# Kernel optimization log

Hardware: AMD Instinct MI355X
Metric: run time of the kernel (lower is better)

Reference implementation:

```python
import jax, jax.numpy as jnp
import numpy as np

# Fixed molemap hierarchy: leaf groups under level-2 nodes 65..72
GROUPS = [(0, 7), (7, 30), (30, 48), (48, 53), (53, 58), (58, 59), (59, 62), (62, 65)]
GROUP_SIZES = [b - a for a, b in GROUPS]
# group index of each leaf (which of nodes 65..72 is its parent)
GIDX = np.repeat(np.arange(8), GROUP_SIZES)
# top branch of each leaf: 0 -> node 73 (leaves 0..52), 1 -> node 74 (leaves 53..64)
TIDX = (np.arange(65) >= 53).astype(np.int32)


def _forward(x):
    # x: [N, 65] leaf logits
    N = x.shape[0]
    # leaf-level probs: softmax of leaf logits within each sibling group (children of 65..72)
    leaf_probs = jnp.concatenate(
        [jax.nn.softmax(x[:, a:b], axis=-1) for a, b in GROUPS], axis=-1
    )  # [N, 65]
    # level-2 node logits = mean of their leaf logits (nodes 65..72)
    means = jnp.stack([x[:, a:b].mean(axis=-1) for a, b in GROUPS], axis=-1)  # [N, 8]
    # level-1 node logits = mean over all leaves beneath (node 73: leaves 0..52, node 74: 53..64)
    m_top = jnp.stack([x[:, :53].mean(axis=-1), x[:, 53:].mean(axis=-1)], axis=-1)  # [N, 2]
    p_top = jax.nn.softmax(m_top, axis=-1)  # [N, 2] -> nodes 73, 74
    # level-2 probs: softmax among siblings (65..68 under 73, 69..72 under 74)
    p_lvl2 = jnp.concatenate(
        [jax.nn.softmax(means[:, :4], axis=-1), jax.nn.softmax(means[:, 4:], axis=-1)],
        axis=-1,
    )  # [N, 8] -> nodes 65..72
    # node_probs layout: [leaves 0..64 | nodes 65..72 | nodes 73..74 | root 75 (=1)]
    node_probs = jnp.concatenate(
        [leaf_probs, p_lvl2, p_top, jnp.ones((N, 1), dtype=x.dtype)], axis=-1
    )  # [N, 76]
    # root-to-leaf path product: p(root)=1 * p(level1) * p(level2) * p(leaf)
    leaf_path_probs = leaf_probs * p_lvl2[:, GIDX] * p_top[:, TIDX]  # [N, 65]
    return leaf_path_probs, node_probs


def setup_inputs() -> dict:
    key = jax.random.key(0)
    x = jax.random.normal(key, (524288, 65), dtype=jnp.float32)
    return {"x": x}


def reference(x):
    return _forward(x)
```

## Files before the change

kernel.cpp:

```cpp
#include <hip/hip_runtime.h>
#include <hip/hip_bf16.h>
#include <math.h>


#define NLEAF 65
#define NNODE 76

__global__ __launch_bounds__(256) void hier_molemap_kernel(
    const float* __restrict__ x,
    float* __restrict__ out_leaf,
    float* __restrict__ out_node,
    int N)
{
    int row = blockIdx.x * blockDim.x + threadIdx.x;
    if (row >= N) return;

    const float* __restrict__ xr = x + (size_t)row * NLEAF;

    float v[NLEAF];
#pragma unroll
    for (int i = 0; i < NLEAF; ++i) v[i] = xr[i];

    constexpr int ga[8] = {0, 7, 30, 48, 53, 58, 59, 62};
    constexpr int gb[8] = {7, 30, 48, 53, 58, 59, 62, 65};

    float gsum[8];
    float means[8];

#pragma unroll
    for (int g = 0; g < 8; ++g) {
        float mx = -INFINITY;
        float sx = 0.0f;
#pragma unroll
        for (int i = ga[g]; i < gb[g]; ++i) {
            mx = fmaxf(mx, v[i]);
            sx += v[i];
        }
        gsum[g] = sx;
        means[g] = sx * (1.0f / (float)(gb[g] - ga[g]));
        float denom = 0.0f;
#pragma unroll
        for (int i = ga[g]; i < gb[g]; ++i) {
            float e = __expf(v[i] - mx);
            v[i] = e;
            denom += e;
        }
        float inv = 1.0f / denom;
#pragma unroll
        for (int i = ga[g]; i < gb[g]; ++i) v[i] *= inv;
    }

    float m0 = (gsum[0] + gsum[1] + gsum[2] + gsum[3]) * (1.0f / 53.0f);
    float m1 = (gsum[4] + gsum[5] + gsum[6] + gsum[7]) * (1.0f / 12.0f);
    float mt = fmaxf(m0, m1);
    float e0 = __expf(m0 - mt);
    float e1 = __expf(m1 - mt);
    float invt = 1.0f / (e0 + e1);
    float pt0 = e0 * invt;
    float pt1 = e1 * invt;

    float p2[8];
    {
        float mxa = fmaxf(fmaxf(means[0], means[1]), fmaxf(means[2], means[3]));
        float sa = 0.0f;
#pragma unroll
        for (int g = 0; g < 4; ++g) { p2[g] = __expf(means[g] - mxa); sa += p2[g]; }
        float inva = 1.0f / sa;
#pragma unroll
        for (int g = 0; g < 4; ++g) p2[g] *= inva;

        float mxb = fmaxf(fmaxf(means[4], means[5]), fmaxf(means[6], means[7]));
        float sb = 0.0f;
#pragma unroll
        for (int g = 4; g < 8; ++g) { p2[g] = __expf(means[g] - mxb); sb += p2[g]; }
        float invb = 1.0f / sb;
#pragma unroll
        for (int g = 4; g < 8; ++g) p2[g] *= invb;
    }

    float* __restrict__ nr = out_node + (size_t)row * NNODE;
#pragma unroll
    for (int i = 0; i < NLEAF; ++i) nr[i] = v[i];
#pragma unroll
    for (int g = 0; g < 8; ++g) nr[NLEAF + g] = p2[g];
    nr[73] = pt0;
    nr[74] = pt1;
    nr[75] = 1.0f;

    float* __restrict__ lr = out_leaf + (size_t)row * NLEAF;
#pragma unroll
    for (int g = 0; g < 8; ++g) {
        float f = p2[g] * ((g < 4) ? pt0 : pt1);
#pragma unroll
        for (int i = ga[g]; i < gb[g]; ++i) lr[i] = v[i] * f;
    }
}

extern "C" void kernel_launch(void* const* d_in, const int* in_sizes, int n_in,
                              void* d_out, int out_size, void* d_ws, size_t ws_size,
                              hipStream_t stream) {
    const float* x = (const float*)d_in[0];
    int N = in_sizes[0] / NLEAF;

    float* out_leaf = (float*)d_out;
    float* out_node = (float*)d_out + (size_t)N * NLEAF;

    int block = 256;
    int grid = (N + block - 1) / block;
    hier_molemap_kernel<<<grid, block, 0, stream>>>(x, out_leaf, out_node, N);
}
```

Measured before the change: 442.4 us.

## Stage row tiles through LDS for coalesced float4 loads and stores

Each block now loads a 128-row tile of input into shared memory with coalesced float4 reads. Each thread computes one row from LDS, then the leaf and node outputs are staged back through LDS and written with coalesced float4 stores. This replaces strided per-thread global accesses (65/76-float row strides), which are poorly coalesced. The cost is extra LDS traffic, several barriers and possible LDS bank conflicts from the stride-65 per-row accesses, along with lower occupancy from about 39 KB of LDS per block.

```diff
diff --git a/kernel.cpp b/kernel.cpp
--- a/kernel.cpp
+++ b/kernel.cpp
@@ -5,62 +5,81 @@
 
 #define NLEAF 65
 #define NNODE 76
+#define ROWS  128
+#define TPB   128
+#define NSTRIDE 77
 
-__global__ __launch_bounds__(256) void hier_molemap_kernel(
+#define NF   (ROWS * NLEAF)
+#define NF4  (NF / 4)
+#define NQ4  (ROWS * (NNODE/4))
+
+__global__ __launch_bounds__(TPB) void hier_molemap_kernel(
     const float* __restrict__ x,
     float* __restrict__ out_leaf,
     float* __restrict__ out_node,
     int N)
 {
-    int row = blockIdx.x * blockDim.x + threadIdx.x;
-    if (row >= N) return;
+    __shared__ float lds[ROWS * NSTRIDE];
 
-    const float* __restrict__ xr = x + (size_t)row * NLEAF;
+    const int tid  = threadIdx.x;
+    const int row0 = blockIdx.x * ROWS;
+    if (row0 >= N) return;
+    const int R    = min(ROWS, N - row0);
+    const bool full = (R == ROWS);
+
+    if (full) {
+        const float4* __restrict__ src4 = (const float4*)(x + (size_t)row0 * NLEAF);
+        float4* lds4 = (float4*)lds;
+#pragma unroll
+        for (int i = 0; i <= NF4 / TPB; ++i) {
+            int idx = tid + i * TPB;
+            if (idx < NF4) lds4[idx] = src4[idx];
+        }
+    } else {
+        const float* __restrict__ src = x + (size_t)row0 * NLEAF;
+        for (int i = tid; i < R * NLEAF; i += TPB) lds[i] = src[i];
+    }
+    __syncthreads();
 
     float v[NLEAF];
-#pragma unroll
-    for (int i = 0; i < NLEAF; ++i) v[i] = xr[i];
+    float p2[8];
+    float pt0 = 0.0f, pt1 = 0.0f;
 
     constexpr int ga[8] = {0, 7, 30, 48, 53, 58, 59, 62};
     constexpr int gb[8] = {7, 30, 48, 53, 58, 59, 62, 65};
 
-    float gsum[8];
-    float means[8];
+    if (tid < R) {
+        const float* __restrict__ r = lds + tid * NLEAF;
+#pragma unroll
+        for (int i = 0; i < NLEAF; ++i) v[i] = r[i];
 
+        float gsum[8], means[8];
 #pragma unroll
-    for (int g = 0; g < 8; ++g) {
-        float mx = -INFINITY;
-        float sx = 0.0f;
+        for (int g = 0; g < 8; ++g) {
+            float mx = -INFINITY, sx = 0.0f;
 #pragma unroll
-        for (int i = ga[g]; i < gb[g]; ++i) {
-            mx = fmaxf(mx, v[i]);
-            sx += v[i];
+            for (int i = ga[g]; i < gb[g]; ++i) { mx = fmaxf(mx, v[i]); sx += v[i]; }
+            gsum[g]  = sx;
+            means[g] = sx * (1.0f / (float)(gb[g] - ga[g]));
+            float denom = 0.0f;
+#pragma unroll
+            for (int i = ga[g]; i < gb[g]; ++i) {
+                float e = __expf(v[i] - mx);
+                v[i] = e;
+                denom += e;
+            }
+            float inv = 1.0f / denom;
+#pragma unroll
+            for (int i = ga[g]; i < gb[g]; ++i) v[i] *= inv;
         }
-        gsum[g] = sx;
-        means[g] = sx * (1.0f / (float)(gb[g] - ga[g]));
-        float denom = 0.0f;
-#pragma unroll
-        for (int i = ga[g]; i < gb[g]; ++i) {
-            float e = __expf(v[i] - mx);
-            v[i] = e;
-            denom += e;
-        }
-        float inv = 1.0f / denom;
-#pragma unroll
-        for (int i = ga[g]; i < gb[g]; ++i) v[i] *= inv;
-    }
 
-    float m0 = (gsum[0] + gsum[1] + gsum[2] + gsum[3]) * (1.0f / 53.0f);
-    float m1 = (gsum[4] + gsum[5] + gsum[6] + gsum[7]) * (1.0f / 12.0f);
-    float mt = fmaxf(m0, m1);
-    float e0 = __expf(m0 - mt);
-    float e1 = __expf(m1 - mt);
-    float invt = 1.0f / (e0 + e1);
-    float pt0 = e0 * invt;
-    float pt1 = e1 * invt;
+        float m0 = (gsum[0] + gsum[1] + gsum[2] + gsum[3]) * (1.0f / 53.0f);
+        float m1 = (gsum[4] + gsum[5] + gsum[6] + gsum[7]) * (1.0f / 12.0f);
+        float mt = fmaxf(m0, m1);
+        float e0 = __expf(m0 - mt), e1 = __expf(m1 - mt);
+        float invt = 1.0f / (e0 + e1);
+        pt0 = e0 * invt; pt1 = e1 * invt;
 
-    float p2[8];
-    {
         float mxa = fmaxf(fmaxf(means[0], means[1]), fmaxf(means[2], means[3]));
         float sa = 0.0f;
 #pragma unroll
@@ -76,23 +95,62 @@
         float invb = 1.0f / sb;
 #pragma unroll
         for (int g = 4; g < 8; ++g) p2[g] *= invb;
+
+        float* __restrict__ w = lds + tid * NLEAF;
+#pragma unroll
+        for (int g = 0; g < 8; ++g) {
+            float f = p2[g] * ((g < 4) ? pt0 : pt1);
+#pragma unroll
+            for (int i = ga[g]; i < gb[g]; ++i) w[i] = v[i] * f;
+        }
     }
+    __syncthreads();
 
-    float* __restrict__ nr = out_node + (size_t)row * NNODE;
+    if (full) {
+        float4* __restrict__ dst4 = (float4*)(out_leaf + (size_t)row0 * NLEAF);
+        const float4* lds4 = (const float4*)lds;
 #pragma unroll
-    for (int i = 0; i < NLEAF; ++i) nr[i] = v[i];
+        for (int i = 0; i <= NF4 / TPB; ++i) {
+            int idx = tid + i * TPB;
+            if (idx < NF4) dst4[idx] = lds4[idx];
+        }
+    } else {
+        float* __restrict__ dst = out_leaf + (size_t)row0 * NLEAF;
+        for (int i = tid; i < R * NLEAF; i += TPB) dst[i] = lds[i];
+    }
+    __syncthreads();
+
+    if (tid < R) {
+        float* __restrict__ nr = lds + tid * NSTRIDE;
 #pragma unroll
-    for (int g = 0; g < 8; ++g) nr[NLEAF + g] = p2[g];
-    nr[73] = pt0;
-    nr[74] = pt1;
-    nr[75] = 1.0f;
+        for (int i = 0; i < NLEAF; ++i) nr[i] = v[i];
+#pragma unroll
+        for (int g = 0; g < 8; ++g) nr[NLEAF + g] = p2[g];
+        nr[73] = pt0;
+        nr[74] = pt1;
+        nr[75] = 1.0f;
+    }
+    __syncthreads();
 
-    float* __restrict__ lr = out_leaf + (size_t)row * NLEAF;
+    if (full) {
+        float4* __restrict__ dst4 = (float4*)(out_node + (size_t)row0 * NNODE);
 #pragma unroll
-    for (int g = 0; g < 8; ++g) {
-        float f = p2[g] * ((g < 4) ? pt0 : pt1);
-#pragma unroll
-        for (int i = ga[g]; i < gb[g]; ++i) lr[i] = v[i] * f;
+        for (int i = 0; i < NQ4 / TPB; ++i) {
+            int q = tid + i * TPB;
+            int r = q / (NNODE / 4);
+            int c = q - r * (NNODE / 4);
+            const float* s = lds + r * NSTRIDE + c * 4;
+            float4 val;
+            val.x = s[0]; val.y = s[1]; val.z = s[2]; val.w = s[3];
+            dst4[q] = val;
+        }
+    } else {
+        float* __restrict__ dst = out_node + (size_t)row0 * NNODE;
+        for (int j = tid; j < R * NNODE; j += TPB) {
+            int r = j / NNODE;
+            int c = j - r * NNODE;
+            dst[j] = lds[r * NSTRIDE + c];
+        }
     }
 }
 
@@ -105,7 +163,6 @@
     float* out_leaf = (float*)d_out;
     float* out_node = (float*)d_out + (size_t)N * NLEAF;
 
-    int block = 256;
-    int grid = (N + block - 1) / block;
-    hier_molemap_kernel<<<grid, block, 0, stream>>>(x, out_leaf, out_node, N);
+    int grid = (N + ROWS - 1) / ROWS;
+    hier_molemap_kernel<<<grid, TPB, 0, stream>>>(x, out_leaf, out_node, N);
 }
```

Result: faster. 394.4 us (-10.8%).
